# Kernel optimization log

Hardware: AMD Instinct MI355X
Metric: run time of the kernel (lower is better)

The kernel has to match this reference:

```python
import jax, jax.numpy as jnp
import numpy as np

N, C_IN, H, W = 32, 128, 56, 56
C_OUT, KH, KW = 256, 3, 3
STRIDE = (1, 1)
PAD = (1, 1)


def setup_inputs() -> dict:
    key = jax.random.key(0)
    k_x, k_w, k_b = jax.random.split(key, 3)
    x = jax.random.normal(k_x, (N, C_IN, H, W), dtype=jnp.float32)
    # kaiming_uniform-like scale for weight, uniform bias in [-1/sqrt(fan_in), 1/sqrt(fan_in)]
    fan_in = C_IN * KH * KW
    bound_w = float(np.sqrt(6.0 / ((1 + 5.0) * fan_in)))  # kaiming_uniform a=sqrt(5)
    weight = jax.random.uniform(k_w, (C_OUT, C_IN, KH, KW), dtype=jnp.float32,
                                minval=-bound_w, maxval=bound_w)
    bound_b = float(1.0 / np.sqrt(fan_in))
    bias = jax.random.uniform(k_b, (C_OUT,), dtype=jnp.float32,
                              minval=-bound_b, maxval=bound_b)
    return {"x": x, "weight": weight, "bias": bias}


def reference(x, weight, bias):
    # Faithful math of the im2col conv: zero padding (ph,pw)=(1,1), stride 1,
    # groups=1 -> identical to a standard cross-correlation conv2d + bias.
    out = jax.lax.conv_general_dilated(
        x, weight,
        window_strides=STRIDE,
        padding=[(PAD[0], PAD[0]), (PAD[1], PAD[1])],
        dimension_numbers=("NCHW", "OIHW", "NCHW"),
    )
    return out + bias[None, :, None, None]
```

## Files before the change

kernel.cpp:

```cpp
#include <hip/hip_runtime.h>


#define NB   32
#define CIN  128
#define HH   56
#define WWD  56
#define COUT 256
#define HWP  3136
#define KTOT 1152
#define HP   58
#define XTN  (HP*HP*CIN)

typedef __bf16 bf16x8 __attribute__((ext_vector_type(8)));
typedef float  f32x4  __attribute__((ext_vector_type(4)));
typedef unsigned short u16;
typedef u16 u16x4 __attribute__((ext_vector_type(4)));
typedef u16 u16x8 __attribute__((ext_vector_type(8)));

__device__ __forceinline__ u16 f2b(float f) {
  unsigned u = __float_as_uint(f);
  u += 0x7fffu + ((u >> 16) & 1u);
  return (u16)(u >> 16);
}

__device__ __forceinline__ void load_lds16(const u16* g, u16* l) {
  __builtin_amdgcn_global_load_lds(
      (const __attribute__((address_space(1))) unsigned int*)g,
      (__attribute__((address_space(3))) unsigned int*)l, 16, 0, 0);
}

__global__ __launch_bounds__(256) void k_transpose_x(const float* __restrict__ x,
                                                     u16* __restrict__ xt) {
  __shared__ u16 tile[64][68];
  const int n  = blockIdx.z;
  const int p0 = blockIdx.x * 64;
  const int c0 = blockIdx.y * 64;
  const int t  = threadIdx.x;

  const float* xp = x + (size_t)n * CIN * HWP + (size_t)c0 * HWP + p0;
  const int pl = (t & 15) * 4;
  const int cr = t >> 4;
#pragma unroll
  for (int j = 0; j < 4; ++j) {
    int c = cr + j * 16;
    f32x4 v = *(const f32x4*)&xp[(size_t)c * HWP + pl];
    u16x4 h;
    h[0] = f2b(v[0]); h[1] = f2b(v[1]); h[2] = f2b(v[2]); h[3] = f2b(v[3]);
    *(u16x4*)&tile[c][pl] = h;
  }
  __syncthreads();
  u16* xb = xt + (size_t)n * XTN + c0;
  const int ch = (t & 7) * 8;
  const int pr = t >> 3;
#pragma unroll
  for (int j = 0; j < 2; ++j) {
    int p  = pr + j * 32;
    int s  = p0 + p;
    int oh = s / WWD;
    int ow = s - oh * WWD;
    u16x8 o;
#pragma unroll
    for (int i = 0; i < 8; ++i) o[i] = tile[ch + i][p];
    *(u16x8*)&xb[((size_t)(oh + 1) * HP + (ow + 1)) * CIN + ch] = o;
  }
}

__global__ __launch_bounds__(256) void k_transform_w(const float* __restrict__ w,
                                                     u16* __restrict__ Wt,
                                                     u16* __restrict__ xt) {
  int o = blockIdx.x * 256 + threadIdx.x;
  if (o < COUT * KTOT) {
    int co  = o / KTOT;
    int rem = o - co * KTOT;
    int kk  = rem >> 7;
    int ci  = rem & 127;
    int kh  = kk / 3;
    int kw  = kk - kh * 3;
    Wt[o] = f2b(w[(((size_t)co * CIN + ci) * 3 + kh) * 3 + kw]);
  }
#pragma unroll
  for (int j = 0; j < 4; ++j) {
    unsigned e = (unsigned)o + j * 294912u;
    if (e < 933888u) {
      unsigned n  = e / 29184u;
      unsigned rm = e - n * 29184u;
      unsigned bp = rm >> 7;
      unsigned ch = rm & 127u;
      unsigned ih, iw;
      if (bp < 58u)       { ih = 0;  iw = bp; }
      else if (bp < 116u) { ih = 57; iw = bp - 58u; }
      else { unsigned c2 = bp - 116u; ih = 1u + (c2 >> 1); iw = (c2 & 1u) ? 57u : 0u; }
      xt[(((size_t)n * HP + ih) * HP + iw) * CIN + ch] = (u16)0;
    }
  }
}


__device__ __forceinline__ int uX_off(int kt) {
  int ksp = kt >> 1;
  int kh  = (ksp >= 6) ? 2 : ((ksp >= 3) ? 1 : 0);
  int kw  = ksp - kh * 3;
  return (kh * HP + kw) * CIN + ((kt & 1) << 6);
}

__global__ __launch_bounds__(256, 2) void k_conv_gemm(
    const u16* __restrict__ xt, const u16* __restrict__ Wt,
    const float* __restrict__ bias, float* __restrict__ out) {
  __shared__ u16 lX[16384];
  __shared__ u16 lW[8192];

  const int tid  = threadIdx.x;
  const int wave = tid >> 6;
  const int lane = tid & 63;

  const int bid  = blockIdx.x;
  const int orig = (bid & 7) * 98 + (bid >> 3);
  const int bx   = orig >> 1;
  const int by   = orig & 1;
  const int m0   = bx * 256;
  const int co0  = by * 128;

  const int r  = lane & 15;
  const int q  = lane >> 4;
  const int r7 = r & 7;
  const int wm = (wave & 1) * 128;
  const int wc = (wave >> 1) * 64;

  const int rsub = lane >> 3;
  const int pso  = ((lane & 7) ^ rsub) * 8;

  int pbX[8], ldoA[8];
#pragma unroll
  for (int c = 0; c < 8; ++c) {
    const int rowb = wave * 64 + c * 8;
    const int m  = m0 + rowb + rsub;
    const int n  = m / HWP;
    const int s  = m - n * HWP;
    const int oh = s / WWD;
    const int ow = s - oh * WWD;
    pbX[c]  = ((n * HP + oh) * HP + ow) * CIN + pso;
    ldoA[c] = rowb * 64;
  }
  int pbW[4], ldoB[4];
#pragma unroll
  for (int c = 0; c < 4; ++c) {
    const int rowb = wave * 32 + c * 8;
    pbW[c]  = (co0 + rowb + rsub) * KTOT + pso;
    ldoB[c] = rowb * 64;
  }
  float bias_r[4];
#pragma unroll
  for (int tj = 0; tj < 4; ++tj) bias_r[tj] = bias[co0 + wc + tj * 16 + r];

  f32x4 acc[8][4];
#pragma unroll
  for (int i = 0; i < 8; ++i)
#pragma unroll
    for (int j = 0; j < 4; ++j) acc[i][j] = (f32x4){0.f, 0.f, 0.f, 0.f};

#pragma unroll 1
  for (int kt = 0; kt < 18; ++kt) {
    const int uxo = uX_off(kt);
    const int uwo = kt * 64;
    __syncthreads();
#pragma unroll
    for (int c = 0; c < 8; ++c)
      load_lds16(xt + pbX[c] + uxo, &lX[ldoA[c]]);
#pragma unroll
    for (int c = 0; c < 4; ++c)
      load_lds16(Wt + pbW[c] + uwo, &lW[ldoB[c]]);
    __syncthreads();

#pragma unroll
    for (int kk = 0; kk < 2; ++kk) {
      const int sw = ((kk * 4 + q) ^ r7) * 8;
      bf16x8 b[4];
#pragma unroll
      for (int tj = 0; tj < 4; ++tj)
        b[tj] = *(const bf16x8*)&lW[(wc + tj * 16 + r) * 64 + sw];
      bf16x8 a[8];
#pragma unroll
      for (int ti = 0; ti < 8; ++ti)
        a[ti] = *(const bf16x8*)&lX[(wm + ti * 16 + r) * 64 + sw];
#pragma unroll
      for (int ti = 0; ti < 8; ++ti)
#pragma unroll
        for (int tj = 0; tj < 4; ++tj)
          acc[ti][tj] = __builtin_amdgcn_mfma_f32_16x16x32_bf16(
              a[ti], b[tj], acc[ti][tj], 0, 0, 0);
    }
  }

#pragma unroll
  for (int ti = 0; ti < 8; ++ti) {
    const int m4 = m0 + wm + ti * 16 + q * 4;
    const int n  = m4 / HWP;
    const int s  = m4 - n * HWP;
    float* op = out + (size_t)n * COUT * HWP + s;
#pragma unroll
    for (int tj = 0; tj < 4; ++tj) {
      const int co = co0 + wc + tj * 16 + r;
      f32x4 v = acc[ti][tj];
      const float bv = bias_r[tj];
      v[0] += bv; v[1] += bv; v[2] += bv; v[3] += bv;
      *(f32x4*)(op + (size_t)co * HWP) = v;
    }
  }
}

extern "C" void kernel_launch(void* const* d_in, const int* in_sizes, int n_in,
                              void* d_out, int out_size, void* d_ws, size_t ws_size,
                              hipStream_t stream) {
  const float* x    = (const float*)d_in[0];
  const float* w    = (const float*)d_in[1];
  const float* bias = (const float*)d_in[2];
  float* out        = (float*)d_out;

  u16* xt = (u16*)d_ws;
  u16* Wt = xt + (size_t)NB * XTN;

  k_transform_w<<<dim3(1152), dim3(256), 0, stream>>>(w, Wt, xt);
  k_transpose_x<<<dim3(49, 2, 32), dim3(256), 0, stream>>>(x, xt);
  k_conv_gemm<<<dim3(784), dim3(256), 0, stream>>>(xt, Wt, bias, out);
}
```

Before: 214.3 us.

## Load activation fragments directly to registers and double-buffer weights in LDS

The GEMM tile changes from 256x128 to 512x64, so each wave owns 128 rows across all 64 output channels. Activation operands are now loaded straight from global memory into registers with a software-pipelined two-set (P/Q) scheme, which removes the activation LDS staging. Weights are double-buffered in LDS with one barrier per k-step, so the next tile's loads overlap the current MFMAs. The cost is more register pressure and uncoalesced, non-LDS-reused global activation loads, and the raw vmcnt waits rely on an assumed instruction order.

```diff
diff --git a/kernel.cpp b/kernel.cpp
--- a/kernel.cpp
+++ b/kernel.cpp
@@ -103,11 +103,24 @@
   return (kh * HP + kw) * CIN + ((kt & 1) << 6);
 }
 
+#define LD_A(SET_, uoff_) do { _Pragma("unroll") \
+  for (int ti = 0; ti < 8; ++ti) \
+    SET_[ti] = *(const bf16x8*)(xt + offA[ti] + (uoff_)); } while (0)
+
+#define RD_W(buf_, kk_) do { _Pragma("unroll") \
+  for (int tj = 0; tj < 4; ++tj) \
+    bf[tj] = *(const bf16x8*)&lW[buf_][(tj * 16 + r) * 64 + (((kk_) * 4 + q) ^ r7) * 8]; } while (0)
+
+#define MFMA_SET(SET_) do { _Pragma("unroll") \
+  for (int ti = 0; ti < 8; ++ti) \
+    { _Pragma("unroll") for (int tj = 0; tj < 4; ++tj) \
+      acc[ti][tj] = __builtin_amdgcn_mfma_f32_16x16x32_bf16( \
+          SET_[ti], bf[tj], acc[ti][tj], 0, 0, 0); } } while (0)
+
 __global__ __launch_bounds__(256, 2) void k_conv_gemm(
     const u16* __restrict__ xt, const u16* __restrict__ Wt,
     const float* __restrict__ bias, float* __restrict__ out) {
-  __shared__ u16 lX[16384];
-  __shared__ u16 lW[8192];
+  __shared__ u16 lW[2][4096];
 
   const int tid  = threadIdx.x;
   const int wave = tid >> 6;
@@ -115,42 +128,39 @@
 
   const int bid  = blockIdx.x;
   const int orig = (bid & 7) * 98 + (bid >> 3);
-  const int bx   = orig >> 1;
-  const int by   = orig & 1;
-  const int m0   = bx * 256;
-  const int co0  = by * 128;
+  const int bx   = orig >> 2;
+  const int by   = orig & 3;
+  const int m0   = bx * 512;
+  const int co0  = by * 64;
 
   const int r  = lane & 15;
   const int q  = lane >> 4;
   const int r7 = r & 7;
-  const int wm = (wave & 1) * 128;
-  const int wc = (wave >> 1) * 64;
-
-  const int rsub = lane >> 3;
-  const int pso  = ((lane & 7) ^ rsub) * 8;
-
-  int pbX[8], ldoA[8];
-#pragma unroll
-  for (int c = 0; c < 8; ++c) {
-    const int rowb = wave * 64 + c * 8;
-    const int m  = m0 + rowb + rsub;
+
+  float bias_r[4];
+#pragma unroll
+  for (int tj = 0; tj < 4; ++tj) bias_r[tj] = bias[co0 + tj * 16 + r];
+
+  int offA[8];
+#pragma unroll
+  for (int ti = 0; ti < 8; ++ti) {
+    const int m  = m0 + wave * 128 + ti * 16 + r;
     const int n  = m / HWP;
     const int s  = m - n * HWP;
     const int oh = s / WWD;
     const int ow = s - oh * WWD;
-    pbX[c]  = ((n * HP + oh) * HP + ow) * CIN + pso;
-    ldoA[c] = rowb * 64;
-  }
-  int pbW[4], ldoB[4];
-#pragma unroll
-  for (int c = 0; c < 4; ++c) {
-    const int rowb = wave * 32 + c * 8;
+    offA[ti] = ((n * HP + oh) * HP + ow) * CIN + q * 8;
+  }
+
+  const int rsub = lane >> 3;
+  const int pso  = ((lane & 7) ^ rsub) * 8;
+  int pbW[2], ldoW[2];
+#pragma unroll
+  for (int c = 0; c < 2; ++c) {
+    const int rowb = wave * 16 + c * 8;
     pbW[c]  = (co0 + rowb + rsub) * KTOT + pso;
-    ldoB[c] = rowb * 64;
-  }
-  float bias_r[4];
-#pragma unroll
-  for (int tj = 0; tj < 4; ++tj) bias_r[tj] = bias[co0 + wc + tj * 16 + r];
+    ldoW[c] = rowb * 64;
+  }
 
   f32x4 acc[8][4];
 #pragma unroll
@@ -158,48 +168,49 @@
 #pragma unroll
     for (int j = 0; j < 4; ++j) acc[i][j] = (f32x4){0.f, 0.f, 0.f, 0.f};
 
+  bf16x8 P[8], Q[8], bf[4];
+
+#pragma unroll
+  for (int c = 0; c < 2; ++c) load_lds16(Wt + pbW[c], &lW[0][ldoW[c]]);
+  LD_A(P, 0);
+  asm volatile("s_waitcnt vmcnt(8)" ::: "memory");
+  __builtin_amdgcn_s_barrier();
+
 #pragma unroll 1
-  for (int kt = 0; kt < 18; ++kt) {
-    const int uxo = uX_off(kt);
-    const int uwo = kt * 64;
-    __syncthreads();
-#pragma unroll
-    for (int c = 0; c < 8; ++c)
-      load_lds16(xt + pbX[c] + uxo, &lX[ldoA[c]]);
-#pragma unroll
-    for (int c = 0; c < 4; ++c)
-      load_lds16(Wt + pbW[c] + uwo, &lW[ldoB[c]]);
-    __syncthreads();
-
-#pragma unroll
-    for (int kk = 0; kk < 2; ++kk) {
-      const int sw = ((kk * 4 + q) ^ r7) * 8;
-      bf16x8 b[4];
-#pragma unroll
-      for (int tj = 0; tj < 4; ++tj)
-        b[tj] = *(const bf16x8*)&lW[(wc + tj * 16 + r) * 64 + sw];
-      bf16x8 a[8];
-#pragma unroll
-      for (int ti = 0; ti < 8; ++ti)
-        a[ti] = *(const bf16x8*)&lX[(wm + ti * 16 + r) * 64 + sw];
-#pragma unroll
-      for (int ti = 0; ti < 8; ++ti)
-#pragma unroll
-        for (int tj = 0; tj < 4; ++tj)
-          acc[ti][tj] = __builtin_amdgcn_mfma_f32_16x16x32_bf16(
-              a[ti], b[tj], acc[ti][tj], 0, 0, 0);
-    }
+  for (int kt = 0; kt < 17; ++kt) {
+    const int cur  = kt & 1;
+    const int uxo  = uX_off(kt);
+    const int uxoN = uX_off(kt + 1);
+#pragma unroll
+    for (int c = 0; c < 2; ++c)
+      load_lds16(Wt + pbW[c] + (kt + 1) * 64, &lW[cur ^ 1][ldoW[c]]);
+    LD_A(Q, uxo + 32);
+    RD_W(cur, 0);
+    MFMA_SET(P);
+    LD_A(P, uxoN);
+    RD_W(cur, 1);
+    MFMA_SET(Q);
+    asm volatile("s_waitcnt vmcnt(8)" ::: "memory");
+    __builtin_amdgcn_s_barrier();
+  }
+  {
+    const int uxo = uX_off(17);
+    LD_A(Q, uxo + 32);
+    RD_W(1, 0);
+    MFMA_SET(P);
+    RD_W(1, 1);
+    MFMA_SET(Q);
   }
 
 #pragma unroll
   for (int ti = 0; ti < 8; ++ti) {
-    const int m4 = m0 + wm + ti * 16 + q * 4;
+    const int m4 = m0 + wave * 128 + ti * 16 + q * 4;
     const int n  = m4 / HWP;
     const int s  = m4 - n * HWP;
     float* op = out + (size_t)n * COUT * HWP + s;
 #pragma unroll
     for (int tj = 0; tj < 4; ++tj) {
-      const int co = co0 + wc + tj * 16 + r;
+      const int co = co0 + tj * 16 + r;
       f32x4 v = acc[ti][tj];
       const float bv = bias_r[tj];
       v[0] += bv; v[1] += bv; v[2] += bv; v[3] += bv;
```

Result: slower. 283.8 us (+32.4%).

## Triple-buffer conv GEMM LDS with 8 waves and ping-pong phased MFMA schedule

Applied to the files above, without the earlier changes.

Restructures the implicit-GEMM conv kernel to use 512 threads (8 waves), a triple-buffered dynamic LDS ring (144 KB), and a two-stage prefetch of K-tiles issued directly to LDS. Each K-step is split into two half-phases that interleave staging loads with MFMA work, using barriers, explicit waitcnt and s_setprio. The aim is to hide global-load latency and remove the full sync-load-sync stall of the old loop. In exchange each wave holds a smaller accumulator tile, the barriers are more intricate, and the large LDS footprint allows only one block per CU despite the launch bound.

```diff
diff --git a/kernel.cpp b/kernel.cpp
--- a/kernel.cpp
+++ b/kernel.cpp
@@ -95,7 +95,6 @@
   }
 }
 
-
 __device__ __forceinline__ int uX_off(int kt) {
   int ksp = kt >> 1;
   int kh  = (ksp >= 6) ? 2 : ((ksp >= 3) ? 1 : 0);
@@ -103,12 +102,27 @@
   return (kh * HP + kw) * CIN + ((kt & 1) << 6);
 }
 
-__global__ __launch_bounds__(256, 2) void k_conv_gemm(
+#define RD_B_PH() do { _Pragma("unroll") for (int kk = 0; kk < 2; ++kk) \
+  { _Pragma("unroll") for (int tj = 0; tj < 2; ++tj) \
+    b[kk][tj] = *(const bf16x8*)&lds[Boff + ((wn + tj * 16 + r) << 6) + (kk ? sw1 : sw0)]; } } while (0)
+
+#define RD_A_PH(qm_) do { _Pragma("unroll") for (int kk = 0; kk < 2; ++kk) \
+  { _Pragma("unroll") for (int ti = 0; ti < 4; ++ti) \
+    a[kk][ti] = *(const bf16x8*)&lds[Aoff + ((wm + (qm_) * 64 + ti * 16 + r) << 6) + (kk ? sw1 : sw0)]; } } while (0)
+
+#define MM_PH(qm_) do { _Pragma("unroll") for (int kk = 0; kk < 2; ++kk) \
+  { _Pragma("unroll") for (int ti = 0; ti < 4; ++ti) \
+    { _Pragma("unroll") for (int tj = 0; tj < 2; ++tj) \
+      acc[(qm_) * 4 + ti][tj] = __builtin_amdgcn_mfma_f32_16x16x32_bf16( \
+          a[kk][ti], b[kk][tj], acc[(qm_) * 4 + ti][tj], 0, 0, 0); } } } while (0)
+
+#define STG_A(c_) load_lds16(xt + pbXc[c_] + ux2, &lds[sAoff + ((c_) << 12) + ldA])
+#define STG_B(c_) load_lds16(Wt + pbWc[c_] + uw2, &lds[sBoff + ((c_) << 12) + ldA])
+
+__global__ __launch_bounds__(512, 2) void k_conv_gemm(
     const u16* __restrict__ xt, const u16* __restrict__ Wt,
     const float* __restrict__ bias, float* __restrict__ out) {
-  __shared__ u16 lX[16384];
-  __shared__ u16 lW[8192];
-
+  extern __shared__ u16 lds[];
   const int tid  = threadIdx.x;
   const int wave = tid >> 6;
   const int lane = tid & 63;
@@ -123,72 +137,113 @@
   const int r  = lane & 15;
   const int q  = lane >> 4;
   const int r7 = r & 7;
-  const int wm = (wave & 1) * 128;
-  const int wc = (wave >> 1) * 64;
+  const int wm = (wave >> 2) * 128;
+  const int wn = (wave & 3) * 32;
+  const int sw0 = (q ^ r7) * 8;
+  const int sw1 = sw0 ^ 32;
 
   const int rsub = lane >> 3;
   const int pso  = ((lane & 7) ^ rsub) * 8;
-
-  int pbX[8], ldoA[8];
-#pragma unroll
-  for (int c = 0; c < 8; ++c) {
-    const int rowb = wave * 64 + c * 8;
-    const int m  = m0 + rowb + rsub;
+  const int ldA  = wave << 9;
+
+  int pbXc[4];
+#pragma unroll
+  for (int c = 0; c < 4; ++c) {
+    const int rowb = c * 64 + wave * 8 + rsub;
+    const int m  = m0 + rowb;
     const int n  = m / HWP;
     const int s  = m - n * HWP;
     const int oh = s / WWD;
     const int ow = s - oh * WWD;
-    pbX[c]  = ((n * HP + oh) * HP + ow) * CIN + pso;
-    ldoA[c] = rowb * 64;
-  }
-  int pbW[4], ldoB[4];
-#pragma unroll
-  for (int c = 0; c < 4; ++c) {
-    const int rowb = wave * 32 + c * 8;
-    pbW[c]  = (co0 + rowb + rsub) * KTOT + pso;
-    ldoB[c] = rowb * 64;
-  }
-  float bias_r[4];
-#pragma unroll
-  for (int tj = 0; tj < 4; ++tj) bias_r[tj] = bias[co0 + wc + tj * 16 + r];
-
-  f32x4 acc[8][4];
+    pbXc[c] = ((n * HP + oh) * HP + ow) * CIN + pso;
+  }
+  int pbWc[2];
+#pragma unroll
+  for (int c = 0; c < 2; ++c)
+    pbWc[c] = (co0 + c * 64 + wave * 8 + rsub) * KTOT + pso;
+
+  float bias_r[2];
+#pragma unroll
+  for (int tj = 0; tj < 2; ++tj) bias_r[tj] = bias[co0 + wn + tj * 16 + r];
+
+  f32x4 acc[8][2];
 #pragma unroll
   for (int i = 0; i < 8; ++i)
 #pragma unroll
-    for (int j = 0; j < 4; ++j) acc[i][j] = (f32x4){0.f, 0.f, 0.f, 0.f};
+    for (int j = 0; j < 2; ++j) acc[i][j] = (f32x4){0.f, 0.f, 0.f, 0.f};
+
+#pragma unroll
+  for (int c = 0; c < 4; ++c) load_lds16(xt + pbXc[c], &lds[(c << 12) + ldA]);
+#pragma unroll
+  for (int c = 0; c < 2; ++c) load_lds16(Wt + pbWc[c], &lds[49152 + (c << 12) + ldA]);
+#pragma unroll
+  for (int c = 0; c < 4; ++c) load_lds16(xt + pbXc[c] + 64, &lds[16384 + (c << 12) + ldA]);
+#pragma unroll
+  for (int c = 0; c < 2; ++c) load_lds16(Wt + pbWc[c] + 64, &lds[57344 + (c << 12) + ldA]);
+  asm volatile("s_waitcnt vmcnt(6)" ::: "memory");
+  __builtin_amdgcn_s_barrier();
+
+  bf16x8 a[2][4], b[2][2];
+  int bA = 0, sA = 2;
 
 #pragma unroll 1
-  for (int kt = 0; kt < 18; ++kt) {
-    const int uxo = uX_off(kt);
-    const int uwo = kt * 64;
-    __syncthreads();
-#pragma unroll
-    for (int c = 0; c < 8; ++c)
-      load_lds16(xt + pbX[c] + uxo, &lX[ldoA[c]]);
-#pragma unroll
-    for (int c = 0; c < 4; ++c)
-      load_lds16(Wt + pbW[c] + uwo, &lW[ldoB[c]]);
-    __syncthreads();
-
-#pragma unroll
-    for (int kk = 0; kk < 2; ++kk) {
-      const int sw = ((kk * 4 + q) ^ r7) * 8;
-      bf16x8 b[4];
-#pragma unroll
-      for (int tj = 0; tj < 4; ++tj)
-        b[tj] = *(const bf16x8*)&lW[(wc + tj * 16 + r) * 64 + sw];
-      bf16x8 a[8];
-#pragma unroll
-      for (int ti = 0; ti < 8; ++ti)
-        a[ti] = *(const bf16x8*)&lX[(wm + ti * 16 + r) * 64 + sw];
-#pragma unroll
-      for (int ti = 0; ti < 8; ++ti)
-#pragma unroll
-        for (int tj = 0; tj < 4; ++tj)
-          acc[ti][tj] = __builtin_amdgcn_mfma_f32_16x16x32_bf16(
-              a[ti], b[tj], acc[ti][tj], 0, 0, 0);
-    }
+  for (int kt = 0; kt < 16; ++kt) {
+    const int Aoff  = bA << 14;
+    const int Boff  = 49152 + (bA << 13);
+    const int sAoff = sA << 14;
+    const int sBoff = 49152 + (sA << 13);
+    const int ux2   = uX_off(kt + 2);
+    const int uw2   = (kt + 2) << 6;
+
+    RD_B_PH(); RD_A_PH(0);
+    STG_A(0); STG_A(1); STG_A(2);
+    __builtin_amdgcn_s_barrier();
+    asm volatile("s_waitcnt lgkmcnt(0)" ::: "memory");
+    __builtin_amdgcn_s_setprio(1);
+    MM_PH(0);
+    __builtin_amdgcn_s_setprio(0);
+    __builtin_amdgcn_s_barrier();
+
+    RD_A_PH(1);
+    STG_A(3); STG_B(0); STG_B(1);
+    asm volatile("s_waitcnt vmcnt(6)" ::: "memory");
+    __builtin_amdgcn_s_barrier();
+    asm volatile("s_waitcnt lgkmcnt(0)" ::: "memory");
+    __builtin_amdgcn_s_setprio(1);
+    MM_PH(1);
+    __builtin_amdgcn_s_setprio(0);
+    __builtin_amdgcn_s_barrier();
+
+    bA = (bA == 2) ? 0 : bA + 1;
+    sA = (sA == 2) ? 0 : sA + 1;
+  }
+
+  {
+    const int Aoff = 1 << 14;
+    const int Boff = 49152 + (1 << 13);
+    RD_B_PH(); RD_A_PH(0);
+    __builtin_amdgcn_s_barrier();
+    asm volatile("s_waitcnt lgkmcnt(0)" ::: "memory");
+    __builtin_amdgcn_s_setprio(1);
+    MM_PH(0);
+    __builtin_amdgcn_s_setprio(0);
+    __builtin_amdgcn_s_barrier();
+    RD_A_PH(1);
+    asm volatile("s_waitcnt vmcnt(0)" ::: "memory");
+    __builtin_amdgcn_s_barrier();
+    asm volatile("s_waitcnt lgkmcnt(0)" ::: "memory");
+    __builtin_amdgcn_s_setprio(1);
+    MM_PH(1);
+    __builtin_amdgcn_s_setprio(0);
+    __builtin_amdgcn_s_barrier();
+  }
+  {
+    const int Aoff = 2 << 14;
+    const int Boff = 49152 + (2 << 13);
+    RD_B_PH(); RD_A_PH(0);
+    MM_PH(0);
+    RD_A_PH(1);
+    MM_PH(1);
   }
 
 #pragma unroll
@@ -198,8 +253,8 @@
     const int s  = m4 - n * HWP;
     float* op = out + (size_t)n * COUT * HWP + s;
 #pragma unroll
-    for (int tj = 0; tj < 4; ++tj) {
-      const int co = co0 + wc + tj * 16 + r;
+    for (int tj = 0; tj < 2; ++tj) {
+      const int co = co0 + wn + tj * 16 + r;
       f32x4 v = acc[ti][tj];
       const float bv = bias_r[tj];
       v[0] += bv; v[1] += bv; v[2] += bv; v[3] += bv;
@@ -219,7 +274,14 @@
   u16* xt = (u16*)d_ws;
   u16* Wt = xt + (size_t)NB * XTN;
 
+  static bool attr_done = false;
+  if (!attr_done) {
+    hipFuncSetAttribute(reinterpret_cast<const void*>(k_conv_gemm),
+                        hipFuncAttributeMaxDynamicSharedMemorySize, 147456);
+    attr_done = true;
+  }
+
   k_transform_w<<<dim3(1152), dim3(256), 0, stream>>>(w, Wt, xt);
   k_transpose_x<<<dim3(49, 2, 32), dim3(256), 0, stream>>>(x, xt);
-  k_conv_gemm<<<dim3(784), dim3(256), 0, stream>>>(xt, Wt, bias, out);
-}
+  k_conv_gemm<<<dim3(784), dim3(512), 147456, stream>>>(xt, Wt, bias, out);
+}
```

Measured after the change: 223.1 us. +4.1%, slower.
